# Performance work log

Hardware: AMD Instinct MI355X
Metric: run time of the kernel (lower is better)

## Reference

```python
import jax, jax.numpy as jnp
import numpy as np

H, D_MODEL, D_K, D_V = 16, 1024, 64, 64
B, S = 4, 2048


def _xavier(key, shape):
    # xavier_uniform over last two dims (matches torch for 3D param: fan per matrix)
    fan_in, fan_out = shape[-2], shape[-1]
    limit = jnp.sqrt(6.0 / (fan_in + fan_out))
    return jax.random.uniform(key, shape, jnp.float32, -limit, limit)


def setup_inputs() -> dict:
    key = jax.random.key(0)
    kq, kk, kv, kwq, kwk, kwv, kwo = jax.random.split(key, 7)
    return {
        "Q": jax.random.normal(kq, (B, S, D_MODEL), jnp.float32),
        "K": jax.random.normal(kk, (B, S, D_MODEL), jnp.float32),
        "V": jax.random.normal(kv, (B, S, D_MODEL), jnp.float32),
        "W_Q": _xavier(kwq, (H, D_MODEL, D_K)),
        "W_K": _xavier(kwk, (H, D_MODEL, D_K)),
        "W_V": _xavier(kwv, (H, D_MODEL, D_V)),
        "W_O": _xavier(kwo, (H * D_V, D_MODEL)),
    }


def reference(Q, K, V, W_Q, W_K, W_V, W_O):
    # Per-head projections (batched over heads instead of Python loop)
    q = jnp.einsum("bsm,hmk->bhsk", Q, W_Q)  # [B,H,S,d_k]
    k = jnp.einsum("bsm,hmk->bhsk", K, W_K)  # [B,H,S,d_k]
    v = jnp.einsum("bsm,hmv->bhsv", V, W_V)  # [B,H,S,d_v]

    scale = 1.0 / jnp.sqrt(jnp.asarray(q.shape[-1], q.dtype))
    scores = jnp.einsum("bhqk,bhsk->bhqs", q, k) * scale  # [B,H,S,S]
    attn = jax.nn.softmax(scores, axis=-1)
    heads = jnp.einsum("bhqs,bhsv->bhqv", attn, v)  # [B,H,S,d_v]

    # concat heads along feature dim: [B,S,H*d_v]
    concat = jnp.transpose(heads, (0, 2, 1, 3)).reshape(Q.shape[0], Q.shape[1], -1)
    return concat @ W_O  # [B,S,d_model]
```

## Files before the change

kernel.cpp:

```cpp
#include <hip/hip_runtime.h>
#include <hip/hip_bf16.h>


typedef __attribute__((ext_vector_type(8))) short short8;
typedef __attribute__((ext_vector_type(4))) float floatx4;
typedef unsigned short u16;

#define NH 16
#define DM 1024
#define DK 64
#define NB 4
#define SS 2048

__device__ inline u16 f2bf(float f) {
    unsigned u = __builtin_bit_cast(unsigned, f);
    return (u16)((u + 0x7fffu + ((u >> 16) & 1u)) >> 16);
}

__device__ inline unsigned pk2(float a, float b) {
    unsigned r;
    asm("v_cvt_pk_bf16_f32 %0, %1, %2" : "=v"(r) : "v"(a), "v"(b));
    return r;
}

__device__ inline uint4 cvt8r(float4 lo, float4 hi) {
    uint4 r;
    r.x = pk2(lo.x, lo.y);
    r.y = pk2(lo.z, lo.w);
    r.z = pk2(hi.x, hi.y);
    r.w = pk2(hi.z, hi.w);
    return r;
}

__global__ __launch_bounds__(256, 2) void proj_gemm(
    const float* __restrict__ X,
    const float* __restrict__ W,
    u16* __restrict__ out) {
    __shared__ u16 a_s[128][38];
    __shared__ u16 b_s[128][38];
    const int mtile = blockIdx.x, ntile = blockIdx.y;
    const int t = threadIdx.x;
    const int w = t >> 6, lane = t & 63, quad = lane >> 4, lr = lane & 15;
    const int wm = w & 1, wn = w >> 1;
    const int ar = t >> 2, ac = (t & 3) * 8;
    const int bk = t >> 3, bn = (t & 7) * 8;

    float4 axl[2], axh[2], bwl[2], bwh[2];
#define PROJ_PREF(kk)                                                          \
    {                                                                          \
        _Pragma("unroll") for (int it = 0; it < 2; it++) {                     \
            const float* ap =                                                  \
                &X[(size_t)(mtile * 128 + ar + 64 * it) * DM + (kk) + ac];     \
            axl[it] = *(const float4*)ap;                                      \
            axh[it] = *(const float4*)(ap + 4);                                \
            const float* bp =                                                  \
                &W[((size_t)(ntile * 2 + it) * DM + (kk) + bk) * DK + bn];     \
            bwl[it] = *(const float4*)bp;                                      \
            bwh[it] = *(const float4*)(bp + 4);                                \
        }                                                                      \
    }

    PROJ_PREF(0);
    floatx4 acc[4][4] = {};
    for (int kki = 0; kki < DM / 32; kki++) {
#pragma unroll
        for (int it = 0; it < 2; it++) {
            *(uint4*)&a_s[ar + 64 * it][ac] = cvt8r(axl[it], axh[it]);
            uint4 wv = cvt8r(bwl[it], bwh[it]);
            alignas(16) u16 tmp[8];
            *(uint4*)tmp = wv;
#pragma unroll
            for (int j = 0; j < 8; j++) b_s[64 * it + bn + j][bk] = tmp[j];
        }
        __syncthreads();
        if (kki + 1 < DM / 32) PROJ_PREF((kki + 1) * 32);
        short8 af[4], bf[4];
#pragma unroll
        for (int i = 0; i < 4; i++)
            af[i] = *(const short8*)&a_s[wm * 64 + i * 16 + lr][quad * 8];
#pragma unroll
        for (int j = 0; j < 4; j++)
            bf[j] = *(const short8*)&b_s[wn * 64 + j * 16 + lr][quad * 8];
#pragma unroll
        for (int i = 0; i < 4; i++)
#pragma unroll
            for (int j = 0; j < 4; j++)
                acc[i][j] = __builtin_amdgcn_mfma_f32_16x16x32_bf16(
                    af[i], bf[j], acc[i][j], 0, 0, 0);
        __syncthreads();
    }
#undef PROJ_PREF

    const int b = (mtile * 128) >> 11;
    const int h = ntile * 2 + wn;
#pragma unroll
    for (int i = 0; i < 4; i++)
#pragma unroll
        for (int j = 0; j < 4; j++)
#pragma unroll
            for (int rg = 0; rg < 4; rg++) {
                int m = mtile * 128 + wm * 64 + i * 16 + quad * 4 + rg;
                int s = m & (SS - 1);
                out[((size_t)(b * NH + h) * SS + s) * DK + j * 16 + lr] =
                    f2bf(acc[i][j][rg]);
            }
}

__global__ __launch_bounds__(256) void transpose_v(
    const u16* __restrict__ src, u16* __restrict__ dst) {
    __shared__ u16 ts[64][70];
    const int bh = blockIdx.x, st = blockIdx.y;
    const int t = threadIdx.x;
    const int r = t >> 3, c0 = (t & 7) * 8;
#pragma unroll
    for (int it = 0; it < 2; it++)
        *(uint4*)&ts[r + 32 * it][c0] =
            *(const uint4*)&src[((size_t)bh * SS + st * 64 + r + 32 * it) * DK + c0];
    __syncthreads();
#pragma unroll
    for (int it = 0; it < 2; it++) {
        int dv = r + 32 * it;
        alignas(16) u16 tmp[8];
#pragma unroll
        for (int j = 0; j < 8; j++) tmp[j] = ts[c0 + j][dv];
        *(uint4*)&dst[((size_t)bh * DK + dv) * SS + st * 64 + c0] = *(uint4*)tmp;
    }
}

#define SWZ(r, c) (((r) << 6) + ((c) ^ (((r) & 7) << 3)))

template <bool VT>
__global__ __launch_bounds__(256, 3) void attn_k(
    const u16* q, const u16* __restrict__ k,
    const u16* __restrict__ v, u16* o) {
    __shared__ u16 k_s[64 * 64];
    __shared__ u16 vt_s[64 * 64];

    const int bh = blockIdx.x, qt = blockIdx.y;
    const int t = threadIdx.x;
    const int w = t >> 6, lane = t & 63, quad = lane >> 4, lr = lane & 15;
    const size_t base = (size_t)bh * SS * DK;
    const size_t tbase = (size_t)bh * DK * SS;

    short8 aq[2][2];
#pragma unroll
    for (int qg = 0; qg < 2; qg++) {
        const size_t qrow =
            base + (size_t)(qt * 128 + w * 32 + qg * 16 + lr) * DK;
        aq[qg][0] = *(const short8*)&q[qrow + quad * 8];
        aq[qg][1] = *(const short8*)&q[qrow + 32 + quad * 8];
    }

    floatx4 o_acc[2][4] = {};
    float l0 = 0.f, l1 = 0.f;
    const int sr = t >> 3, sd = (t & 7) * 8;

    const float C1 = 0.18033688f;

    for (int kt = 0; kt < SS / 64; kt++) {
#pragma unroll
        for (int it = 0; it < 2; it++) {
            int r = sr + 32 * it;
            *(uint4*)&k_s[SWZ(r, sd)] =
                *(const uint4*)&k[base + (size_t)(kt * 64 + r) * DK + sd];
            if (VT) {
                *(uint4*)&vt_s[SWZ(r, sd)] =
                    *(const uint4*)&v[tbase + (size_t)r * SS + kt * 64 + sd];
            } else {
                uint4 vv = *(const uint4*)&v[base + (size_t)(kt * 64 + r) * DK + sd];
                alignas(16) u16 tmp[8];
                *(uint4*)tmp = vv;
#pragma unroll
                for (int j = 0; j < 8; j++) vt_s[SWZ(sd + j, r)] = tmp[j];
            }
        }
        __syncthreads();

        floatx4 s0[4] = {}, s1[4] = {};
#pragma unroll
        for (int ks = 0; ks < 2; ks++)
#pragma unroll
            for (int nt = 0; nt < 4; nt++) {
                short8 af =
                    *(const short8*)&k_s[SWZ(nt * 16 + lr, ks * 32 + quad * 8)];
                s0[nt] = __builtin_amdgcn_mfma_f32_16x16x32_bf16(
                    af, aq[0][ks], s0[nt], 0, 0, 0);
                s1[nt] = __builtin_amdgcn_mfma_f32_16x16x32_bf16(
                    af, aq[1][ks], s1[nt], 0, 0, 0);
            }

        unsigned W0[4][2], W1[4][2];
#pragma unroll
        for (int nt = 0; nt < 4; nt++) {
            float p0 = __builtin_amdgcn_exp2f(s0[nt][0] * C1);
            float p1 = __builtin_amdgcn_exp2f(s0[nt][1] * C1);
            float p2 = __builtin_amdgcn_exp2f(s0[nt][2] * C1);
            float p3 = __builtin_amdgcn_exp2f(s0[nt][3] * C1);
            l0 += (p0 + p1) + (p2 + p3);
            W0[nt][0] = pk2(p0, p1);
            W0[nt][1] = pk2(p2, p3);
            float q0 = __builtin_amdgcn_exp2f(s1[nt][0] * C1);
            float q1 = __builtin_amdgcn_exp2f(s1[nt][1] * C1);
            float q2 = __builtin_amdgcn_exp2f(s1[nt][2] * C1);
            float q3 = __builtin_amdgcn_exp2f(s1[nt][3] * C1);
            l1 += (q0 + q1) + (q2 + q3);
            W1[nt][0] = pk2(q0, q1);
            W1[nt][1] = pk2(q2, q3);
        }

        uint4 bf0[2], bf1[2];
#pragma unroll
        for (int ks = 0; ks < 2; ks++) {
            unsigned a0 = W0[2 * ks][0], b0 = W0[2 * ks + 1][0];
            unsigned a1 = W0[2 * ks][1], b1 = W0[2 * ks + 1][1];
            asm("v_permlane32_swap_b32 %0, %1" : "+v"(a0), "+v"(b0));
            asm("v_permlane16_swap_b32 %0, %1" : "+v"(a0), "+v"(b0));
            asm("v_permlane32_swap_b32 %0, %1" : "+v"(a1), "+v"(b1));
            asm("v_permlane16_swap_b32 %0, %1" : "+v"(a1), "+v"(b1));
            bf0[ks].x = a0; bf0[ks].y = a1; bf0[ks].z = b0; bf0[ks].w = b1;
            unsigned c0 = W1[2 * ks][0], d0 = W1[2 * ks + 1][0];
            unsigned c1 = W1[2 * ks][1], d1 = W1[2 * ks + 1][1];
            asm("v_permlane32_swap_b32 %0, %1" : "+v"(c0), "+v"(d0));
            asm("v_permlane16_swap_b32 %0, %1" : "+v"(c0), "+v"(d0));
            asm("v_permlane32_swap_b32 %0, %1" : "+v"(c1), "+v"(d1));
            asm("v_permlane16_swap_b32 %0, %1" : "+v"(c1), "+v"(d1));
            bf1[ks].x = c0; bf1[ks].y = c1; bf1[ks].z = d0; bf1[ks].w = d1;
        }

#pragma unroll
        for (int ks = 0; ks < 2; ks++) {
            short8 p0f = __builtin_bit_cast(short8, bf0[ks]);
            short8 p1f = __builtin_bit_cast(short8, bf1[ks]);
#pragma unroll
            for (int nt = 0; nt < 4; nt++) {
                short8 afv =
                    *(const short8*)&vt_s[SWZ(nt * 16 + lr, ks * 32 + quad * 8)];
                o_acc[0][nt] = __builtin_amdgcn_mfma_f32_16x16x32_bf16(
                    afv, p0f, o_acc[0][nt], 0, 0, 0);
                o_acc[1][nt] = __builtin_amdgcn_mfma_f32_16x16x32_bf16(
                    afv, p1f, o_acc[1][nt], 0, 0, 0);
            }
        }
        __syncthreads();
    }

    l0 += __shfl_xor(l0, 16);
    l0 += __shfl_xor(l0, 32);
    l1 += __shfl_xor(l1, 16);
    l1 += __shfl_xor(l1, 32);
    float inv0 = 1.0f / l0, inv1 = 1.0f / l1;

    const size_t orow0 = base + (size_t)(qt * 128 + w * 32 + lr) * DK;
    const size_t orow1 = orow0 + (size_t)16 * DK;
#pragma unroll
    for (int nt = 0; nt < 4; nt++) {
        uint2 pk;
        pk.x = pk2(o_acc[0][nt][0] * inv0, o_acc[0][nt][1] * inv0);
        pk.y = pk2(o_acc[0][nt][2] * inv0, o_acc[0][nt][3] * inv0);
        *(uint2*)&o[orow0 + nt * 16 + quad * 4] = pk;
        pk.x = pk2(o_acc[1][nt][0] * inv1, o_acc[1][nt][1] * inv1);
        pk.y = pk2(o_acc[1][nt][2] * inv1, o_acc[1][nt][3] * inv1);
        *(uint2*)&o[orow1 + nt * 16 + quad * 4] = pk;
    }
}

__global__ __launch_bounds__(256, 2) void oproj(
    const u16* __restrict__ heads,
    const float* __restrict__ WO,
    float* __restrict__ out) {
    __shared__ u16 a_s[128][38];
    __shared__ u16 b_s[128][38];
    const int mtile = blockIdx.x, ntile = blockIdx.y;
    const int t = threadIdx.x;
    const int w = t >> 6, lane = t & 63, quad = lane >> 4, lr = lane & 15;
    const int wm = w & 1, wn = w >> 1;
    const int ar = t >> 2, ac = (t & 3) * 8;
    const int bk = t >> 3, bn = (t & 7) * 8;
    const int b = (mtile * 128) >> 11;

    uint4 areg[2];
    float4 bwl[2], bwh[2];
#define OP_PREF(kk)                                                            \
    {                                                                          \
        const int h = (kk) >> 6, dvb = (kk) & 63;                              \
        _Pragma("unroll") for (int it = 0; it < 2; it++) {                     \
            int m = mtile * 128 + ar + 64 * it, s = m & (SS - 1);              \
            areg[it] = *(const uint4*)                                         \
                &heads[((size_t)(b * NH + h) * SS + s) * DK + dvb + ac];       \
            const float* bp =                                                  \
                &WO[(size_t)((kk) + bk) * DM + ntile * 128 + 64 * it + bn];    \
            bwl[it] = *(const float4*)bp;                                      \
            bwh[it] = *(const float4*)(bp + 4);                                \
        }                                                                      \
    }

    OP_PREF(0);
    floatx4 acc[4][4] = {};
    for (int kki = 0; kki < DM / 32; kki++) {
#pragma unroll
        for (int it = 0; it < 2; it++) {
            *(uint4*)&a_s[ar + 64 * it][ac] = areg[it];
            uint4 wv = cvt8r(bwl[it], bwh[it]);
            alignas(16) u16 tmp[8];
            *(uint4*)tmp = wv;
#pragma unroll
            for (int j = 0; j < 8; j++) b_s[64 * it + bn + j][bk] = tmp[j];
        }
        __syncthreads();
        if (kki + 1 < DM / 32) OP_PREF((kki + 1) * 32);
        short8 af[4], bf[4];
#pragma unroll
        for (int i = 0; i < 4; i++)
            af[i] = *(const short8*)&a_s[wm * 64 + i * 16 + lr][quad * 8];
#pragma unroll
        for (int j = 0; j < 4; j++)
            bf[j] = *(const short8*)&b_s[wn * 64 + j * 16 + lr][quad * 8];
#pragma unroll
        for (int i = 0; i < 4; i++)
#pragma unroll
            for (int j = 0; j < 4; j++)
                acc[i][j] = __builtin_amdgcn_mfma_f32_16x16x32_bf16(
                    af[i], bf[j], acc[i][j], 0, 0, 0);
        __syncthreads();
    }
#undef OP_PREF

#pragma unroll
    for (int i = 0; i < 4; i++)
#pragma unroll
        for (int j = 0; j < 4; j++)
#pragma unroll
            for (int rg = 0; rg < 4; rg++) {
                int m = mtile * 128 + wm * 64 + i * 16 + quad * 4 + rg;
                int n = ntile * 128 + wn * 64 + j * 16 + lr;
                out[(size_t)m * DM + n] = acc[i][j][rg];
            }
}

extern "C" void kernel_launch(void* const* d_in, const int* in_sizes, int n_in,
                              void* d_out, int out_size, void* d_ws, size_t ws_size,
                              hipStream_t stream) {
    const float* Q  = (const float*)d_in[0];
    const float* K  = (const float*)d_in[1];
    const float* V  = (const float*)d_in[2];
    const float* WQ = (const float*)d_in[3];
    const float* WK = (const float*)d_in[4];
    const float* WV = (const float*)d_in[5];
    const float* WO = (const float*)d_in[6];
    float* out = (float*)d_out;

    char* ws = (char*)d_ws;
    const size_t NQKV = (size_t)NB * NH * SS * DK;
    u16* qp  = (u16*)ws;           ws += NQKV * 2;
    u16* kp  = (u16*)ws;           ws += NQKV * 2;
    u16* vp  = (u16*)ws;           ws += NQKV * 2;
    u16* vtp = (u16*)ws;
    u16* hp  = qp;
    const bool vt_ok = ws_size >= 4 * NQKV * 2;

    dim3 pg(NB * SS / 128, DM / 128);
    proj_gemm<<<pg, 256, 0, stream>>>(Q, WQ, qp);
    proj_gemm<<<pg, 256, 0, stream>>>(K, WK, kp);
    proj_gemm<<<pg, 256, 0, stream>>>(V, WV, vp);

    if (vt_ok) {
        transpose_v<<<dim3(NB * NH, SS / 64), 256, 0, stream>>>(vp, vtp);
        attn_k<true><<<dim3(NB * NH, SS / 128), 256, 0, stream>>>(qp, kp, vtp, hp);
    } else {
        attn_k<false><<<dim3(NB * NH, SS / 128), 256, 0, stream>>>(qp, kp, vp, hp);
    }

    oproj<<<dim3(NB * SS / 128, DM / 128), 256, 0, stream>>>(hp, WO, out);
}
```

Before: 412.8 us.

## Pre-pack weights to bf16 MFMA layout and batch QKV projections in one launch

Adds a prep kernel that converts W_Q/W_K/W_V and W_O to bf16 in a fragment-ready layout, so the projection GEMMs load B operands straight from global memory into registers instead of converting and staging them through shared memory. The three QKV projections are merged into a single launch with a z-dimension, and new 64-row tile GEMM kernels replace the old ones on the main path. Attention occupancy hint is raised from 3 to 4 waves. The weights are repacked on every call, which costs extra kernel launches and memory traffic, and direct B loads from global memory may be less coalesced.

Result: faster. 340.9 us (-17.4%).

```diff
diff --git a/kernel.cpp b/kernel.cpp
--- a/kernel.cpp
+++ b/kernel.cpp
@@ -30,6 +30,172 @@
     r.z = pk2(hi.x, hi.y);
     r.w = pk2(hi.z, hi.w);
     return r;
+}
+
+__global__ __launch_bounds__(256) void prep_w(
+    const float* __restrict__ W0, const float* __restrict__ W1,
+    const float* __restrict__ W2, const float* __restrict__ WO,
+    uint4* __restrict__ dst, int mode) {
+    int idx = blockIdx.x * 256 + threadIdx.x;
+    const int total = mode ? 128 * 1024 : 3 * 16 * 128 * 64;
+    const int stride = gridDim.x * 256;
+    for (; idx < total; idx += stride) {
+        float v[8];
+        if (mode == 0) {
+            int n64 = idx & 63, kt = (idx >> 6) & 127;
+            int h = (idx >> 13) & 15, w = idx >> 17;
+            const float* src = (w == 0 ? W0 : (w == 1 ? W1 : W2)) +
+                               ((size_t)(h * 1024 + kt * 8)) * 64 + n64;
+#pragma unroll
+            for (int j = 0; j < 8; j++) v[j] = src[(size_t)j * 64];
+        } else {
+            int n = idx & 1023, kt = idx >> 10;
+            const float* src = WO + (size_t)(kt * 8) * 1024 + n;
+#pragma unroll
+            for (int j = 0; j < 8; j++) v[j] = src[(size_t)j * 1024];
+        }
+        uint4 r;
+        r.x = pk2(v[0], v[1]);
+        r.y = pk2(v[2], v[3]);
+        r.z = pk2(v[4], v[5]);
+        r.w = pk2(v[6], v[7]);
+        dst[idx] = r;
+    }
+}
+
+__global__ __launch_bounds__(256, 4) void proj_pre(
+    const float* __restrict__ X0, const float* __restrict__ X1,
+    const float* __restrict__ X2, const uint4* __restrict__ wb,
+    u16* __restrict__ outb) {
+    __shared__ u16 a_s[64][40];
+    const int z = blockIdx.z;
+    const float* X = z == 0 ? X0 : (z == 1 ? X1 : X2);
+    u16* out = outb + (size_t)z * ((size_t)NB * NH * SS * DK);
+    const int mtile = blockIdx.x, ntile = blockIdx.y;
+    const int t = threadIdx.x;
+    const int w = t >> 6, lane = t & 63, quad = lane >> 4, lr = lane & 15;
+    const int ar = t >> 2, ac = (t & 3) * 8;
+    const int h = ntile * 2 + (w >> 1);
+    const int nh = (w & 1) * 32;
+    const size_t bbase = (((size_t)z * 16 + h) * 128 + quad) * 64 + nh + lr;
+
+    float4 axl, axh;
+#define PPREFA(kk)                                                             \
+    {                                                                          \
+        const float* ap = &X[(size_t)(mtile * 64 + ar) * DM + (kk) + ac];      \
+        axl = *(const float4*)ap;                                              \
+        axh = *(const float4*)(ap + 4);                                        \
+    }
+    PPREFA(0);
+    uint4 bcur[2], bnx[2];
+    bcur[0] = wb[bbase];
+    bcur[1] = wb[bbase + 16];
+    floatx4 acc[4][2] = {};
+    for (int kki = 0; kki < DM / 32; kki++) {
+        *(uint4*)&a_s[ar][ac] = cvt8r(axl, axh);
+        __syncthreads();
+        if (kki + 1 < DM / 32) {
+            PPREFA((kki + 1) * 32);
+            const size_t bi = bbase + (size_t)(kki + 1) * 4 * 64;
+            bnx[0] = wb[bi];
+            bnx[1] = wb[bi + 16];
+        }
+        short8 af[4];
+#pragma unroll
+        for (int i = 0; i < 4; i++)
+            af[i] = *(const short8*)&a_s[i * 16 + lr][quad * 8];
+#pragma unroll
+        for (int i = 0; i < 4; i++)
+#pragma unroll
+            for (int j = 0; j < 2; j++)
+                acc[i][j] = __builtin_amdgcn_mfma_f32_16x16x32_bf16(
+                    af[i], __builtin_bit_cast(short8, bcur[j]), acc[i][j],
+                    0, 0, 0);
+        __syncthreads();
+        if (kki + 1 < DM / 32) {
+            bcur[0] = bnx[0];
+            bcur[1] = bnx[1];
+        }
+    }
+#undef PPREFA
+
+    const int b = (mtile * 64) >> 11;
+#pragma unroll
+    for (int i = 0; i < 4; i++)
+#pragma unroll
+        for (int j = 0; j < 2; j++)
+#pragma unroll
+            for (int rg = 0; rg < 4; rg++) {
+                int m = mtile * 64 + i * 16 + quad * 4 + rg;
+                int s = m & (SS - 1);
+                out[((size_t)(b * NH + h) * SS + s) * DK + nh + j * 16 + lr] =
+                    f2bf(acc[i][j][rg]);
+            }
+}
+
+__global__ __launch_bounds__(256, 4) void oproj_pre(
+    const u16* __restrict__ heads,
+    const uint4* __restrict__ wob,
+    float* __restrict__ out) {
+    __shared__ u16 a_s[64][40];
+    const int mtile = blockIdx.x, ntile = blockIdx.y;
+    const int t = threadIdx.x;
+    const int w = t >> 6, lane = t & 63, quad = lane >> 4, lr = lane & 15;
+    const int ar = t >> 2, ac = (t & 3) * 8;
+    const int b = (mtile * 64) >> 11;
+    const int nb = ntile * 128 + w * 32;
+    const size_t bbase = (size_t)quad * 1024 + nb + lr;
+
+    uint4 areg;
+#define OPREFA(kk)                                                             \
+    {                                                                          \
+        const int hh = (kk) >> 6, dvb = (kk) & 63;                             \
+        int m = mtile * 64 + ar, s = m & (SS - 1);                             \
+        areg = *(const uint4*)&heads[((size_t)(b * NH + hh) * SS + s) * DK +   \
+                                     dvb + ac];                                \
+    }
+    OPREFA(0);
+    uint4 bcur[2], bnx[2];
+    bcur[0] = wob[bbase];
+    bcur[1] = wob[bbase + 16];
+    floatx4 acc[4][2] = {};
+    for (int kki = 0; kki < DM / 32; kki++) {
+        *(uint4*)&a_s[ar][ac] = areg;
+        __syncthreads();
+        if (kki + 1 < DM / 32) {
+            OPREFA((kki + 1) * 32);
+            const size_t bi = bbase + (size_t)(kki + 1) * 4 * 1024;
+            bnx[0] = wob[bi];
+            bnx[1] = wob[bi + 16];
+        }
+        short8 af[4];
+#pragma unroll
+        for (int i = 0; i < 4; i++)
+            af[i] = *(const short8*)&a_s[i * 16 + lr][quad * 8];
+#pragma unroll
+        for (int i = 0; i < 4; i++)
+#pragma unroll
+            for (int j = 0; j < 2; j++)
+                acc[i][j] = __builtin_amdgcn_mfma_f32_16x16x32_bf16(
+                    af[i], __builtin_bit_cast(short8, bcur[j]), acc[i][j],
+                    0, 0, 0);
+        __syncthreads();
+        if (kki + 1 < DM / 32) {
+            bcur[0] = bnx[0];
+            bcur[1] = bnx[1];
+        }
+    }
+#undef OPREFA
+
+#pragma unroll
+    for (int i = 0; i < 4; i++)
+#pragma unroll
+        for (int j = 0; j < 2; j++)
+#pragma unroll
+            for (int rg = 0; rg < 4; rg++) {
+                int m = mtile * 64 + i * 16 + quad * 4 + rg;
+                out[(size_t)m * DM + nb + j * 16 + lr] = acc[i][j][rg];
+            }
 }
 
 __global__ __launch_bounds__(256, 2) void proj_gemm(
@@ -130,7 +296,7 @@
 #define SWZ(r, c) (((r) << 6) + ((c) ^ (((r) & 7) << 3)))
 
 template <bool VT>
-__global__ __launch_bounds__(256, 3) void attn_k(
+__global__ __launch_bounds__(256, 4) void attn_k(
     const u16* q, const u16* __restrict__ k,
     const u16* __restrict__ v, u16* o) {
     __shared__ u16 k_s[64 * 64];
@@ -351,24 +517,40 @@
 
     char* ws = (char*)d_ws;
     const size_t NQKV = (size_t)NB * NH * SS * DK;
-    u16* qp  = (u16*)ws;           ws += NQKV * 2;
-    u16* kp  = (u16*)ws;           ws += NQKV * 2;
-    u16* vp  = (u16*)ws;           ws += NQKV * 2;
-    u16* vtp = (u16*)ws;
+    const size_t SZ = NQKV * 2;
+    u16* qp  = (u16*)ws;
+    u16* kp  = (u16*)(ws + SZ);
+    u16* vp  = (u16*)(ws + 2 * SZ);
+    u16* vtp = (u16*)(ws + 3 * SZ);
     u16* hp  = qp;
-    const bool vt_ok = ws_size >= 4 * NQKV * 2;
-
-    dim3 pg(NB * SS / 128, DM / 128);
-    proj_gemm<<<pg, 256, 0, stream>>>(Q, WQ, qp);
-    proj_gemm<<<pg, 256, 0, stream>>>(K, WK, kp);
-    proj_gemm<<<pg, 256, 0, stream>>>(V, WV, vp);
-
-    if (vt_ok) {
+
+    const size_t WB_SZ  = 3ull * 16 * 128 * 64 * sizeof(uint4);
+    const size_t WOB_SZ = 128ull * 1024 * sizeof(uint4);
+    const bool tierA = ws_size >= 4 * SZ + WB_SZ + WOB_SZ;
+    const bool tierB = !tierA && ws_size >= 4 * SZ;
+
+    if (tierA || tierB) {
+        uint4* wb  = tierA ? (uint4*)(ws + 4 * SZ) : (uint4*)vtp;
+        uint4* wob = tierA ? (uint4*)(ws + 4 * SZ + WB_SZ) : (uint4*)kp;
+
+        prep_w<<<1536, 256, 0, stream>>>(WQ, WK, WV, WO, wb, 0);
+        if (tierA) prep_w<<<512, 256, 0, stream>>>(WQ, WK, WV, WO, wob, 1);
+
+        proj_pre<<<dim3(NB * SS / 64, DM / 128, 3), 256, 0, stream>>>(
+            Q, K, V, wb, qp);
         transpose_v<<<dim3(NB * NH, SS / 64), 256, 0, stream>>>(vp, vtp);
-        attn_k<true><<<dim3(NB * NH, SS / 128), 256, 0, stream>>>(qp, kp, vtp, hp);
+        attn_k<true><<<dim3(NB * NH, SS / 128), 256, 0, stream>>>(
+            qp, kp, vtp, hp);
+        if (tierB) prep_w<<<512, 256, 0, stream>>>(WQ, WK, WV, WO, wob, 1);
+        oproj_pre<<<dim3(NB * SS / 64, DM / 128), 256, 0, stream>>>(
+            hp, wob, out);
     } else {
-        attn_k<false><<<dim3(NB * NH, SS / 128), 256, 0, stream>>>(qp, kp, vp, hp);
-    }
-
-    oproj<<<dim3(NB * SS / 128, DM / 128), 256, 0, stream>>>(hp, WO, out);
-}
+        dim3 pg(NB * SS / 128, DM / 128);
+        proj_gemm<<<pg, 256, 0, stream>>>(Q, WQ, qp);
+        proj_gemm<<<pg, 256, 0, stream>>>(K, WK, kp);
+        proj_gemm<<<pg, 256, 0, stream>>>(V, WV, vp);
+        attn_k<false><<<dim3(NB * NH, SS / 128), 256, 0, stream>>>(
+            qp, kp, vp, hp);
+        oproj<<<dim3(NB * SS / 128, DM / 128), 256, 0, stream>>>(hp, WO, out);
+    }
+}
```

## Pre-convert inputs and weights to bf16 and use LDS-direct-load GEMMs

Applied to the files above, without the earlier changes.

Adds prep kernels that convert each activation tensor and the transposed weights to bf16 in workspace, using the output buffer and dead Q/K buffers as scratch. New projection and output GEMMs load tiles straight into LDS with global_load_lds and use a swizzled block order for L2 locality. The aim is to cut fp32 read traffic and register staging in the GEMMs. It also raises attention occupancy bounds from 3 to 4 and adds extra conversion launches and memory passes.

Result: faster. 377.8 us (-8.5%).

```diff
diff --git a/kernel.cpp b/kernel.cpp
--- a/kernel.cpp
+++ b/kernel.cpp
@@ -30,6 +30,179 @@
     r.z = pk2(hi.x, hi.y);
     r.w = pk2(hi.z, hi.w);
     return r;
+}
+
+__device__ inline void gload_lds16(const void* g, void* l) {
+    __builtin_amdgcn_global_load_lds(
+        (const __attribute__((address_space(1))) unsigned*)g,
+        (__attribute__((address_space(3))) unsigned*)l, 16, 0, 0);
+}
+
+__global__ __launch_bounds__(256) void prep_x(
+    const float* __restrict__ X, u16* __restrict__ xb) {
+    const int total = NB * SS * DM / 8;
+    int idx = blockIdx.x * 256 + threadIdx.x;
+    const int stride = gridDim.x * 256;
+    for (; idx < total; idx += stride) {
+        const float* p = X + (size_t)idx * 8;
+        float4 lo = *(const float4*)p;
+        float4 hi = *(const float4*)(p + 4);
+        *(uint4*)&xb[(size_t)idx * 8] = cvt8r(lo, hi);
+    }
+}
+
+__global__ __launch_bounds__(256) void prep_w(
+    const float* __restrict__ W0, const float* __restrict__ W1,
+    const float* __restrict__ W2, const float* __restrict__ WO,
+    uint4* __restrict__ dst, int mode) {
+    int idx = blockIdx.x * 256 + threadIdx.x;
+    const int total = mode ? 1024 * 128 : 3 * 1024 * 128;
+    const int stride = gridDim.x * 256;
+    for (; idx < total; idx += stride) {
+        float v[8];
+        if (mode == 0) {
+            int k8 = idx & 127, n = (idx >> 7) & 1023, z = idx >> 17;
+            int h = n >> 6, d = n & 63;
+            const float* src = (z == 0 ? W0 : (z == 1 ? W1 : W2)) +
+                               ((size_t)(h * 1024 + k8 * 8)) * 64 + d;
+#pragma unroll
+            for (int j = 0; j < 8; j++) v[j] = src[(size_t)j * 64];
+        } else {
+            int k8 = idx & 127, n = idx >> 7;
+            const float* src = WO + (size_t)(k8 * 8) * 1024 + n;
+#pragma unroll
+            for (int j = 0; j < 8; j++) v[j] = src[(size_t)j * 1024];
+        }
+        uint4 r;
+        r.x = pk2(v[0], v[1]);
+        r.y = pk2(v[2], v[3]);
+        r.z = pk2(v[4], v[5]);
+        r.w = pk2(v[6], v[7]);
+        dst[idx] = r;
+    }
+}
+
+__global__ __launch_bounds__(256, 2) void gemm_proj(
+    const u16* __restrict__ A, const u16* __restrict__ BT,
+    u16* __restrict__ out) {
+    __shared__ u16 a_s[128 * 32];
+    __shared__ u16 b_s[128 * 32];
+    const int bid = blockIdx.x;
+    const int work = (bid & 7) * 64 + (bid >> 3);
+    const int mtile = work >> 3, ntile = work & 7;
+    const int t = threadIdx.x;
+    const int w = t >> 6, lane = t & 63, quad = lane >> 4, lr = lane & 15;
+    const int wm = w & 1, wn = w >> 1;
+    const int srow = lane >> 2, scol = (lane & 3) * 8;
+
+    const size_t abase =
+        ((size_t)(mtile * 128 + w * 32 + srow)) * DM + scol;
+    const size_t bbase =
+        ((size_t)(ntile * 128 + w * 32 + srow)) * DM + scol;
+    u16* a_dst0 = &a_s[(w * 32) * 32];
+    u16* a_dst1 = &a_s[(w * 32 + 16) * 32];
+    u16* b_dst0 = &b_s[(w * 32) * 32];
+    u16* b_dst1 = &b_s[(w * 32 + 16) * 32];
+
+    floatx4 acc[4][4] = {};
+    for (int kk = 0; kk < DM / 32; kk++) {
+        const size_t ko = (size_t)kk * 32;
+        gload_lds16(A + abase + ko, a_dst0);
+        gload_lds16(A + abase + (size_t)16 * DM + ko, a_dst1);
+        gload_lds16(BT + bbase + ko, b_dst0);
+        gload_lds16(BT + bbase + (size_t)16 * DM + ko, b_dst1);
+        __syncthreads();
+        short8 af[4], bf[4];
+#pragma unroll
+        for (int i = 0; i < 4; i++)
+            af[i] = *(const short8*)&a_s[(wm * 64 + i * 16 + lr) * 32 + quad * 8];
+#pragma unroll
+        for (int j = 0; j < 4; j++)
+            bf[j] = *(const short8*)&b_s[(wn * 64 + j * 16 + lr) * 32 + quad * 8];
+#pragma unroll
+        for (int i = 0; i < 4; i++)
+#pragma unroll
+            for (int j = 0; j < 4; j++)
+                acc[i][j] = __builtin_amdgcn_mfma_f32_16x16x32_bf16(
+                    af[i], bf[j], acc[i][j], 0, 0, 0);
+        __syncthreads();
+    }
+
+    const int b = (mtile * 128) >> 11;
+#pragma unroll
+    for (int i = 0; i < 4; i++)
+#pragma unroll
+        for (int j = 0; j < 4; j++)
+#pragma unroll
+            for (int rg = 0; rg < 4; rg++) {
+                int m = mtile * 128 + wm * 64 + i * 16 + quad * 4 + rg;
+                int s = m & (SS - 1);
+                int n = ntile * 128 + wn * 64 + j * 16 + lr;
+                int h = n >> 6, d = n & 63;
+                out[((size_t)(b * NH + h) * SS + s) * DK + d] =
+                    f2bf(acc[i][j][rg]);
+            }
+}
+
+__global__ __launch_bounds__(256, 2) void gemm_oproj(
+    const u16* __restrict__ heads, const u16* __restrict__ BT,
+    float* __restrict__ out) {
+    __shared__ u16 a_s[128 * 32];
+    __shared__ u16 b_s[128 * 32];
+    const int bid = blockIdx.x;
+    const int work = (bid & 7) * 64 + (bid >> 3);
+    const int mtile = work >> 3, ntile = work & 7;
+    const int t = threadIdx.x;
+    const int w = t >> 6, lane = t & 63, quad = lane >> 4, lr = lane & 15;
+    const int wm = w & 1, wn = w >> 1;
+    const int srow = lane >> 2, scol = (lane & 3) * 8;
+
+    const int b = (mtile * 128) >> 11;
+    const int s0 = (mtile * 128) & (SS - 1);
+    const size_t bbase =
+        ((size_t)(ntile * 128 + w * 32 + srow)) * DM + scol;
+    u16* a_dst0 = &a_s[(w * 32) * 32];
+    u16* a_dst1 = &a_s[(w * 32 + 16) * 32];
+    u16* b_dst0 = &b_s[(w * 32) * 32];
+    u16* b_dst1 = &b_s[(w * 32 + 16) * 32];
+
+    floatx4 acc[4][4] = {};
+    for (int kk = 0; kk < DM / 32; kk++) {
+        const size_t hb =
+            ((size_t)(b * NH + (kk >> 1)) * SS + s0 + w * 32 + srow) * DK +
+            (kk & 1) * 32 + scol;
+        gload_lds16(heads + hb, a_dst0);
+        gload_lds16(heads + hb + (size_t)16 * DK, a_dst1);
+        const size_t ko = (size_t)kk * 32;
+        gload_lds16(BT + bbase + ko, b_dst0);
+        gload_lds16(BT + bbase + (size_t)16 * DM + ko, b_dst1);
+        __syncthreads();
+        short8 af[4], bf[4];
+#pragma unroll
+        for (int i = 0; i < 4; i++)
+            af[i] = *(const short8*)&a_s[(wm * 64 + i * 16 + lr) * 32 + quad * 8];
+#pragma unroll
+        for (int j = 0; j < 4; j++)
+            bf[j] = *(const short8*)&b_s[(wn * 64 + j * 16 + lr) * 32 + quad * 8];
+#pragma unroll
+        for (int i = 0; i < 4; i++)
+#pragma unroll
+            for (int j = 0; j < 4; j++)
+                acc[i][j] = __builtin_amdgcn_mfma_f32_16x16x32_bf16(
+                    af[i], bf[j], acc[i][j], 0, 0, 0);
+        __syncthreads();
+    }
+
+#pragma unroll
+    for (int i = 0; i < 4; i++)
+#pragma unroll
+        for (int j = 0; j < 4; j++)
+#pragma unroll
+            for (int rg = 0; rg < 4; rg++) {
+                int m = mtile * 128 + wm * 64 + i * 16 + quad * 4 + rg;
+                int n = ntile * 128 + wn * 64 + j * 16 + lr;
+                out[(size_t)m * DM + n] = acc[i][j][rg];
+            }
 }
 
 __global__ __launch_bounds__(256, 2) void proj_gemm(
@@ -130,7 +303,7 @@
 #define SWZ(r, c) (((r) << 6) + ((c) ^ (((r) & 7) << 3)))
 
 template <bool VT>
-__global__ __launch_bounds__(256, 3) void attn_k(
+__global__ __launch_bounds__(256, 4) void attn_k(
     const u16* q, const u16* __restrict__ k,
     const u16* __restrict__ v, u16* o) {
     __shared__ u16 k_s[64 * 64];
@@ -351,24 +524,42 @@
 
     char* ws = (char*)d_ws;
     const size_t NQKV = (size_t)NB * NH * SS * DK;
-    u16* qp  = (u16*)ws;           ws += NQKV * 2;
-    u16* kp  = (u16*)ws;           ws += NQKV * 2;
-    u16* vp  = (u16*)ws;           ws += NQKV * 2;
-    u16* vtp = (u16*)ws;
+    const size_t SZ = NQKV * 2;
+    u16* qp  = (u16*)ws;
+    u16* kp  = (u16*)(ws + SZ);
+    u16* vp  = (u16*)(ws + 2 * SZ);
+    u16* vtp = (u16*)(ws + 3 * SZ);
     u16* hp  = qp;
-    const bool vt_ok = ws_size >= 4 * NQKV * 2;
-
-    dim3 pg(NB * SS / 128, DM / 128);
-    proj_gemm<<<pg, 256, 0, stream>>>(Q, WQ, qp);
-    proj_gemm<<<pg, 256, 0, stream>>>(K, WK, kp);
-    proj_gemm<<<pg, 256, 0, stream>>>(V, WV, vp);
-
-    if (vt_ok) {
+
+    const size_t WBT_SZ = 3ull * 1024 * 1024 * 2;
+    const bool ok = ws_size >= 4 * SZ && (size_t)out_size >= WBT_SZ;
+
+    if (ok) {
+        u16* xb = vtp;
+        uint4* wbT  = (uint4*)d_out;
+        uint4* wobT = (uint4*)kp;
+
+        prep_w<<<1536, 256, 0, stream>>>(WQ, WK, WV, WO, wbT, 0);
+
+        const float* Xz[3] = {Q, K, V};
+        for (int z = 0; z < 3; z++) {
+            prep_x<<<2048, 256, 0, stream>>>(Xz[z], xb);
+            gemm_proj<<<512, 256, 0, stream>>>(
+                xb, (const u16*)wbT + (size_t)z * 1024 * 1024,
+                qp + (size_t)z * NQKV);
+        }
         transpose_v<<<dim3(NB * NH, SS / 64), 256, 0, stream>>>(vp, vtp);
-        attn_k<true><<<dim3(NB * NH, SS / 128), 256, 0, stream>>>(qp, kp, vtp, hp);
+        attn_k<true><<<dim3(NB * NH, SS / 128), 256, 0, stream>>>(
+            qp, kp, vtp, hp);
+        prep_w<<<512, 256, 0, stream>>>(WQ, WK, WV, WO, wobT, 1);
+        gemm_oproj<<<512, 256, 0, stream>>>(hp, (const u16*)wobT, out);
     } else {
-        attn_k<false><<<dim3(NB * NH, SS / 128), 256, 0, stream>>>(qp, kp, vp, hp);
-    }
-
-    oproj<<<dim3(NB * SS / 128, DM / 128), 256, 0, stream>>>(hp, WO, out);
-}
+        dim3 pg(NB * SS / 128, DM / 128);
+        proj_gemm<<<pg, 256, 0, stream>>>(Q, WQ, qp);
+        proj_gemm<<<pg, 256, 0, stream>>>(K, WK, kp);
+        proj_gemm<<<pg, 256, 0, stream>>>(V, WV, vp);
+        attn_k<false><<<dim3(NB * NH, SS / 128), 256, 0, stream>>>(
+            qp, kp, vp, hp);
+        oproj<<<dim3(NB * SS / 128, DM / 128), 256, 0, stream>>>(hp, WO, out);
+    }
+}
```
